# Optimization experiments

Measured on AMD Instinct MI355X. Metric: run time of the kernel, lower is better.

The kernel has to match this reference:

```python
import jax, jax.numpy as jnp
import numpy as np

N = 100000   # nodes
E = 1600000  # edges (avg degree 16)
D = 64       # feature dim
LN_EPS = 1e-5


def setup_inputs() -> dict:
    key = jax.random.key(0)
    ks = jax.random.split(key, 12)
    s = 1.0 / np.sqrt(D)
    x = jax.random.normal(ks[0], (N, D), dtype=jnp.float32)
    edge_index = jax.random.randint(ks[1], (2, E), 0, N, dtype=jnp.int32)
    routing_factor = jax.random.uniform(ks[2], (E,), dtype=jnp.float32)
    return {
        "x": x,
        "edge_index": edge_index,
        "routing_factor": routing_factor,
        "W_phys": jax.random.normal(ks[3], (D, D), dtype=jnp.float32) * s,
        "W_neur": jax.random.normal(ks[4], (D, D), dtype=jnp.float32) * s,
        "att_w": jax.random.normal(ks[5], (2 * D,), dtype=jnp.float32) * s,
        "channel_fusion": jnp.float32(0.5),
        "mlp_w1": jax.random.normal(ks[6], (2 * D, D), dtype=jnp.float32) * s,
        "mlp_b1": jnp.zeros((2 * D,), dtype=jnp.float32),
        "mlp_w2": jax.random.normal(ks[7], (D, 2 * D), dtype=jnp.float32) / np.sqrt(2 * D),
        "mlp_b2": jnp.zeros((D,), dtype=jnp.float32),
        "ln1_g": jnp.ones((D,), dtype=jnp.float32),
        "ln1_b": jnp.zeros((D,), dtype=jnp.float32),
        "ln2_g": jnp.ones((D,), dtype=jnp.float32),
        "ln2_b": jnp.zeros((D,), dtype=jnp.float32),
    }


def _layernorm(h, g, b):
    mu = jnp.mean(h, axis=-1, keepdims=True)
    var = jnp.var(h, axis=-1, keepdims=True)
    return (h - mu) * jax.lax.rsqrt(var + LN_EPS) * g + b


def reference(x, edge_index, routing_factor, W_phys, W_neur, att_w,
              channel_fusion, mlp_w1, mlp_b1, mlp_w2, mlp_b2,
              ln1_g, ln1_b, ln2_g, ln2_b):
    src, dst = edge_index[0], edge_index[1]
    x_src = x[src]  # [E, D]
    # att(cat([x_src, x_dst])) == x_src @ w[:D] + x_dst @ w[D:]
    att_scores = x_src @ att_w[:D] + x[dst] @ att_w[D:]  # [E]
    # segment softmax over destination nodes (equivalent to per-node loop)
    seg_max = jax.ops.segment_max(att_scores, dst, num_segments=N)
    e = jnp.exp(att_scores - seg_max[dst])
    denom = jax.ops.segment_sum(e, dst, num_segments=N)
    att = e / denom[dst]  # [E]
    # dual-channel messages (dropout inactive at eval)
    phys = routing_factor[:, None] * (x_src @ W_phys.T)
    neur = x_src @ W_neur.T
    alpha = jax.nn.sigmoid(channel_fusion)
    messages = att[:, None] * (alpha * phys + (1.0 - alpha) * neur)  # [E, D]
    out = jax.ops.segment_sum(messages, dst, num_segments=N)  # [N, D]
    h = _layernorm(jax.nn.gelu(out, approximate=False) + x, ln1_g, ln1_b)
    m = jax.nn.gelu(h @ mlp_w1.T + mlp_b1, approximate=False) @ mlp_w2.T + mlp_b2
    return _layernorm(m + h, ln2_g, ln2_b)
```

## Files before the change

kernel.cpp:

```cpp
#include <hip/hip_runtime.h>
#include <math.h>

#define NN 100000
#define NE 1600000
#define DD 64
#define NBUK 782
#define TILE 8192
#define NTB ((NE + TILE - 1) / TILE)
#define BSTRIDE 3072
#define SCAP 3072

typedef __attribute__((ext_vector_type(8))) short short8;
typedef __attribute__((ext_vector_type(4))) float f32x4;
typedef __attribute__((ext_vector_type(4))) _Float16 h4;

__device__ __forceinline__ float gelu_exact(float v) {
    return 0.5f * v * (1.0f + erff(v * 0.7071067811865475f));
}

__device__ __forceinline__ unsigned short f2bf(float f) {
    unsigned u = __float_as_uint(f);
    return (unsigned short)((u + 0x7FFFu + ((u >> 16) & 1u)) >> 16);
}
__device__ __forceinline__ float bf2f(unsigned short h) {
    return __uint_as_float((unsigned)h << 16);
}
__device__ __forceinline__ void split8v(float4 x0, float4 x1, short8& hi, short8& lo) {
    float v[8] = {x0.x, x0.y, x0.z, x0.w, x1.x, x1.y, x1.z, x1.w};
    #pragma unroll
    for (int i = 0; i < 8; ++i) {
        unsigned short h = f2bf(v[i]);
        hi[i] = (short)h;
        lo[i] = (short)f2bf(v[i] - bf2f(h));
    }
}
__device__ __forceinline__ void lds_frag(const float* g, int row, int u0, int s,
                                         short8& hi, short8& lo) {
    float4 p0 = *(const float4*)&g[row * 64 + ((u0 ^ s) << 2)];
    float4 p1 = *(const float4*)&g[row * 64 + (((u0 + 1) ^ s) << 2)];
    split8v(p0, p1, hi, lo);
}

template<bool F16>
__global__ __launch_bounds__(256) void k01(
    const float* __restrict__ Wp, const float* __restrict__ Wn,
    const float* __restrict__ w1, const float* __restrict__ w2,
    const float* __restrict__ cf,
    unsigned short* __restrict__ wh, unsigned short* __restrict__ wl,
    const float* __restrict__ x, const float* __restrict__ attw,
    float* __restrict__ es1, _Float16* __restrict__ xh)
{
    if (blockIdx.x < 96) {
        int t = blockIdx.x * 256 + threadIdx.x;
        float alpha = 1.0f / (1.0f + __expf(-cf[0]));
        float beta  = 1.0f - alpha;
        float v;
        if (t < 8192) {
            int d = t >> 7, k = t & 127;
            v = (k < 64) ? alpha * Wp[d * 64 + k] : beta * Wn[d * 64 + (k - 64)];
        } else if (t < 16384) {
            v = w1[t - 8192];
        } else {
            v = w2[t - 16384];
        }
        unsigned short h = f2bf(v);
        wh[t] = h;
        wl[t] = f2bf(v - bf2f(h));
    } else {
        int n = (blockIdx.x - 96) * 256 + threadIdx.x;
        if (n >= NN) return;
        const float4* x4 = (const float4*)(x + (size_t)n * DD);
        float a = 0.f;
        #pragma unroll
        for (int i = 0; i < DD/4; ++i) {
            float4 v = x4[i];
            a += v.x*attw[4*i+0] + v.y*attw[4*i+1] + v.z*attw[4*i+2] + v.w*attw[4*i+3];
            if (F16) {
                h4 hv = {(_Float16)v.x, (_Float16)v.y, (_Float16)v.z, (_Float16)v.w};
                *(h4*)(xh + (size_t)n * DD + 4*i) = hv;
            }
        }
        es1[n] = __expf(a);
    }
}

__global__ __launch_bounds__(1024) void ks_bscan(
    const int* __restrict__ bcount, int* __restrict__ bbase)
{
    __shared__ int sa[1024], sb[1024];
    int t = threadIdx.x;
    int v = (t < NBUK) ? bcount[t] : 0;
    sa[t] = v;
    __syncthreads();
    int* s = sa; int* d = sb;
    #pragma unroll
    for (int o = 1; o < 1024; o <<= 1) {
        d[t] = s[t] + ((t >= o) ? s[t - o] : 0);
        __syncthreads();
        int* tmp = s; s = d; d = tmp;
    }
    if (t < NBUK) bbase[t] = s[t] - v;
    if (t == 0) bbase[NBUK] = NE;
}

__global__ __launch_bounds__(256) void kscat1(
    const int* __restrict__ ei, const float* __restrict__ rf,
    int* __restrict__ bcount, uint2* __restrict__ tmp)
{
    __shared__ int hist[NBUK];
    __shared__ int gbase[NBUK];
    for (int i = threadIdx.x; i < NBUK; i += 256) hist[i] = 0;
    __syncthreads();
    int base = blockIdx.x * TILE;
    int end  = min(base + TILE, NE);
    for (int e = base + threadIdx.x; e < end; e += 256)
        atomicAdd(&hist[ei[NE + e] >> 7], 1);
    __syncthreads();
    for (int i = threadIdx.x; i < NBUK; i += 256) {
        int c = hist[i];
        gbase[i] = c ? (i * BSTRIDE + atomicAdd(bcount + i, c)) : 0;
        hist[i] = 0;
    }
    __syncthreads();
    for (int e = base + threadIdx.x; e < end; e += 256) {
        int src = ei[e];
        int dst = ei[NE + e];
        int b = dst >> 7;
        int t = atomicAdd(&hist[b], 1);
        tmp[gbase[b] + t] =
            make_uint2((unsigned)src | ((unsigned)(dst & 127) << 17),
                       __float_as_uint(rf[e]));
    }
}

__global__ __launch_bounds__(256) void kscat2(
    const uint2* __restrict__ tmp, const int* __restrict__ bcount,
    const int* __restrict__ bbase,
    int* __restrict__ off, uint2* __restrict__ sorted)
{
    __shared__ int hist[128], scn[128], tick[128];
    __shared__ uint2 obuf[SCAP];
    int b   = blockIdx.x;
    int tid = threadIdx.x;
    int si = b * BSTRIDE;
    int so = bbase[b];
    int m  = bcount[b];

    if (tid < 128) { hist[tid] = 0; tick[tid] = 0; }
    __syncthreads();

    for (int i = tid; i < m; i += 256)
        atomicAdd(&hist[tmp[si + i].x >> 17], 1);
    __syncthreads();

    if (tid < 128) scn[tid] = hist[tid];
    __syncthreads();
    #pragma unroll
    for (int o = 1; o < 128; o <<= 1) {
        int v = (tid < 128 && tid >= o) ? scn[tid - o] : 0;
        __syncthreads();
        if (tid < 128) scn[tid] += v;
        __syncthreads();
    }

    int nb0 = b * 128;
    if (tid < 128 && nb0 + tid < NN) off[nb0 + tid] = so + scn[tid] - hist[tid];
    if (b == NBUK - 1 && tid == 0) off[NN] = NE;
    __syncthreads();

    for (int i = tid; i < m; i += 256) {
        uint2 pr = tmp[si + i];
        int l = pr.x >> 17;
        int t = atomicAdd(&tick[l], 1);
        int lp = (scn[l] - hist[l]) + t;
        uint2 val = make_uint2(pr.x & 0x1FFFFu, pr.y);
        if (lp < SCAP) obuf[lp] = val;
        else sorted[so + lp] = val;
    }
    __syncthreads();
    int mm = min(m, SCAP);
    for (int i = tid; i < mm; i += 256)
        sorted[so + i] = obuf[i];
}

template<bool F16>
__global__ __launch_bounds__(256) void k4a_agg(
    const float2* __restrict__ sorted, const int* __restrict__ off,
    const float* __restrict__ es1,
    const float* __restrict__ x, const _Float16* __restrict__ xh,
    float* __restrict__ uv)
{
    int lane = threadIdx.x & 63;
    int n = blockIdx.x * 4 + (threadIdx.x >> 6);
    int r0 = off[n], r1 = off[n + 1];

    float den = 0.f, u = 0.f, v = 0.f;
    for (int base = r0; base < r1; base += 64) {
        int idx = base + lane;
        int cnt = min(64, r1 - base);
        int srcl = 0; float el = 0.f, efl = 0.f;
        if (idx < r1) {
            float2 p = sorted[idx];
            srcl = __float_as_int(p.x);
            el   = es1[srcl];
            efl  = el * p.y;
        }
        int j = 0;
        for (; j + 8 <= cnt; j += 8) {
            int a[8]; float e[8], f[8];
            #pragma unroll
            for (int t = 0; t < 8; ++t) {
                a[t] = __shfl(srcl, j + t);
                e[t] = __shfl(el,   j + t);
                f[t] = __shfl(efl,  j + t);
            }
            float xv[8];
            #pragma unroll
            for (int t = 0; t < 8; ++t)
                xv[t] = F16 ? (float)xh[(size_t)a[t] * DD + lane]
                            : x[(size_t)a[t] * DD + lane];
            #pragma unroll
            for (int t = 0; t < 8; ++t) {
                den += e[t];
                v += e[t] * xv[t];
                u += f[t] * xv[t];
            }
        }
        for (; j < cnt; ++j) {
            int   sj = __shfl(srcl, j);
            float ej = __shfl(el,   j);
            float fj = __shfl(efl,  j);
            float xv = F16 ? (float)xh[(size_t)sj * DD + lane]
                           : x[(size_t)sj * DD + lane];
            den += ej;
            v += ej * xv;
            u += fj * xv;
        }
    }
    float inv = (r1 > r0) ? 1.f / den : 0.f;
    uv[(size_t)n * 2*DD + lane]      = u * inv;
    uv[(size_t)n * 2*DD + DD + lane] = v * inv;
}

__global__ __launch_bounds__(512, 4) void k4b5(
    const float* __restrict__ uv,
    const unsigned short* __restrict__ wh, const unsigned short* __restrict__ wl,
    const float* __restrict__ x,
    const float* __restrict__ g1, const float* __restrict__ be1,
    const float* __restrict__ bb1, const float* __restrict__ bb2,
    const float* __restrict__ g2, const float* __restrict__ be2,
    float* __restrict__ out)
{
    __shared__ unsigned short WH[8192], WL[8192];
    __shared__ unsigned short W2H[4096], W2L[4096];
    __shared__ float Gt[8][1024];

    int tid  = threadIdx.x;
    int lane = tid & 63;
    int wv   = tid >> 6;
    int quad = lane >> 4, l16 = lane & 15;
    int s7   = l16 & 7;
    int nb = blockIdx.x * 128 + wv * 16;
    float* gt = Gt[wv];

    const float4* arow4 = (const float4*)(uv + (size_t)min(nb + l16, NN - 1) * 128);
    float4 av[8];
    #pragma unroll
    for (int ks = 0; ks < 4; ++ks) {
        av[2*ks]   = arow4[ks*8 + quad*2];
        av[2*ks+1] = arow4[ks*8 + quad*2 + 1];
    }
    float xr[4][4];
    #pragma unroll
    for (int r = 0; r < 4; ++r) {
        size_t nld = (size_t)min(nb + quad*4 + r, NN - 1) * 64;
        #pragma unroll
        for (int nt = 0; nt < 4; ++nt) xr[r][nt] = x[nld + nt*16 + l16];
    }

    #pragma unroll
    for (int k = 0; k < 2; ++k) {
        int i = tid + k*512;
        int row = i >> 4, u = i & 15;
        int up = u ^ (row & 7);
        *(short8*)&WH[row*128 + up*8] = *(const short8*)&wh[i*8];
        *(short8*)&WL[row*128 + up*8] = *(const short8*)&wl[i*8];
    }
    __syncthreads();

    f32x4 acc0[4] = {};
    #pragma unroll
    for (int ks = 0; ks < 4; ++ks) {
        short8 ah, al;
        split8v(av[2*ks], av[2*ks+1], ah, al);
        int u0 = 4*ks + quad;
        #pragma unroll
        for (int nt = 0; nt < 4; ++nt) {
            int wo = (nt*16 + l16)*128 + (u0 ^ s7)*8;
            short8 bh = *(const short8*)&WH[wo];
            short8 bl = *(const short8*)&WL[wo];
            acc0[nt] = __builtin_amdgcn_mfma_f32_16x16x32_bf16(ah, bh, acc0[nt], 0, 0, 0);
            acc0[nt] = __builtin_amdgcn_mfma_f32_16x16x32_bf16(al, bh, acc0[nt], 0, 0, 0);
            acc0[nt] = __builtin_amdgcn_mfma_f32_16x16x32_bf16(ah, bl, acc0[nt], 0, 0, 0);
        }
    }

    float hn[4][4];
    #pragma unroll
    for (int r = 0; r < 4; ++r) {
        float hv[4];
        #pragma unroll
        for (int nt = 0; nt < 4; ++nt)
            hv[nt] = gelu_exact(acc0[nt][r]) + xr[r][nt];
        float s = hv[0] + hv[1] + hv[2] + hv[3];
        #pragma unroll
        for (int o = 1; o < 16; o <<= 1) s += __shfl_xor(s, o);
        float mu = s * (1.0f/64.0f);
        float q = 0.f;
        #pragma unroll
        for (int nt = 0; nt < 4; ++nt) { float t = hv[nt] - mu; q += t*t; }
        #pragma unroll
        for (int o = 1; o < 16; o <<= 1) q += __shfl_xor(q, o);
        float rs = rsqrtf(q * (1.0f/64.0f) + 1e-5f);
        int row = quad*4 + r;
        #pragma unroll
        for (int nt = 0; nt < 4; ++nt) {
            int c = nt*16 + l16;
            float h = (hv[nt] - mu) * rs * g1[c] + be1[c];
            hn[r][nt] = h;
            int u = c >> 2;
            gt[row*64 + ((u ^ (row & 7)) << 2) + (c & 3)] = h;
        }
    }
    __syncthreads();

    #pragma unroll
    for (int k = 0; k < 2; ++k) {
        int i = tid + k*512;
        int row = i >> 3, u = i & 7;
        int up = u ^ (row & 7);
        *(short8*)&WH[row*64 + up*8] = *(const short8*)&wh[8192 + i*8];
        *(short8*)&WL[row*64 + up*8] = *(const short8*)&wl[8192 + i*8];
    }
    {
        int row = tid >> 3, u = tid & 7;
        int up = u ^ (row & 7);
        *(short8*)&W2H[row*64 + up*8] = *(const short8*)&wh[16384 + row*128 + u*8];
        *(short8*)&W2L[row*64 + up*8] = *(const short8*)&wl[16384 + row*128 + u*8];
    }
    __syncthreads();

    short8 ah1[2], al1[2];
    #pragma unroll
    for (int ks = 0; ks < 2; ++ks)
        lds_frag(gt, l16, 8*ks + 2*quad, s7, ah1[ks], al1[ks]);

    f32x4 acc2[4] = {};
    #pragma unroll
    for (int half = 0; half < 2; ++half) {
        f32x4 a1[4] = {};
        #pragma unroll
        for (int ks = 0; ks < 2; ++ks) {
            int u0 = 4*ks + quad;
            #pragma unroll
            for (int t = 0; t < 4; ++t) {
                int row = half*64 + t*16 + l16;
                int wo = row*64 + ((u0 ^ s7))*8;
                short8 bh = *(const short8*)&WH[wo];
                short8 bl = *(const short8*)&WL[wo];
                a1[t] = __builtin_amdgcn_mfma_f32_16x16x32_bf16(ah1[ks], bh, a1[t], 0, 0, 0);
                a1[t] = __builtin_amdgcn_mfma_f32_16x16x32_bf16(al1[ks], bh, a1[t], 0, 0, 0);
                a1[t] = __builtin_amdgcn_mfma_f32_16x16x32_bf16(ah1[ks], bl, a1[t], 0, 0, 0);
            }
        }
        #pragma unroll
        for (int t = 0; t < 4; ++t) {
            float b1v = bb1[half*64 + t*16 + l16];
            #pragma unroll
            for (int r = 0; r < 4; ++r) {
                int row = quad*4 + r;
                int c = t*16 + l16;
                int u = c >> 2;
                gt[row*64 + ((u ^ (row & 7)) << 2) + (c & 3)] = gelu_exact(a1[t][r] + b1v);
            }
        }
        #pragma unroll
        for (int ks2 = 0; ks2 < 2; ++ks2) {
            short8 ah2, al2;
            lds_frag(gt, l16, 8*ks2 + 2*quad, s7, ah2, al2);
            int u0 = 4*ks2 + quad;
            #pragma unroll
            for (int nt2 = 0; nt2 < 4; ++nt2) {
                int wo = (nt2*16 + l16)*64 + (u0 ^ s7)*8;
                short8 bh = *(const short8*)&W2H[wo];
                short8 bl = *(const short8*)&W2L[wo];
                acc2[nt2] = __builtin_amdgcn_mfma_f32_16x16x32_bf16(ah2, bh, acc2[nt2], 0, 0, 0);
                acc2[nt2] = __builtin_amdgcn_mfma_f32_16x16x32_bf16(al2, bh, acc2[nt2], 0, 0, 0);
                acc2[nt2] = __builtin_amdgcn_mfma_f32_16x16x32_bf16(ah2, bl, acc2[nt2], 0, 0, 0);
            }
        }
        if (half == 0) {
            __syncthreads();
            int row = tid >> 3, u = tid & 7;
            int up = u ^ (row & 7);
            *(short8*)&W2H[row*64 + up*8] = *(const short8*)&wh[16384 + row*128 + 64 + u*8];
            *(short8*)&W2L[row*64 + up*8] = *(const short8*)&wl[16384 + row*128 + 64 + u*8];
            __syncthreads();
        }
    }

    #pragma unroll
    for (int r = 0; r < 4; ++r) {
        int n = nb + quad * 4 + r;
        float mv[4];
        #pragma unroll
        for (int nt = 0; nt < 4; ++nt)
            mv[nt] = acc2[nt][r] + hn[r][nt] + bb2[nt*16 + l16];
        float s = mv[0] + mv[1] + mv[2] + mv[3];
        #pragma unroll
        for (int o = 1; o < 16; o <<= 1) s += __shfl_xor(s, o);
        float mu = s * (1.0f/64.0f);
        float q = 0.f;
        #pragma unroll
        for (int nt = 0; nt < 4; ++nt) { float t = mv[nt] - mu; q += t*t; }
        #pragma unroll
        for (int o = 1; o < 16; o <<= 1) q += __shfl_xor(q, o);
        float rs = rsqrtf(q * (1.0f/64.0f) + 1e-5f);
        if (n < NN) {
            #pragma unroll
            for (int nt = 0; nt < 4; ++nt) {
                int c = nt*16 + l16;
                out[(size_t)n * 64 + c] = (mv[nt] - mu) * rs * g2[c] + be2[c];
            }
        }
    }
}

extern "C" void kernel_launch(void* const* d_in, const int* in_sizes, int n_in,
                              void* d_out, int out_size, void* d_ws, size_t ws_size,
                              hipStream_t stream) {
    const float* x    = (const float*)d_in[0];
    const int*   ei   = (const int*)d_in[1];
    const float* rf   = (const float*)d_in[2];
    const float* Wp   = (const float*)d_in[3];
    const float* Wn   = (const float*)d_in[4];
    const float* attw = (const float*)d_in[5];
    const float* cf   = (const float*)d_in[6];
    const float* w1   = (const float*)d_in[7];
    const float* b1   = (const float*)d_in[8];
    const float* w2   = (const float*)d_in[9];
    const float* b2   = (const float*)d_in[10];
    const float* g1   = (const float*)d_in[11];
    const float* be1  = (const float*)d_in[12];
    const float* g2   = (const float*)d_in[13];
    const float* be2  = (const float*)d_in[14];
    float* out = (float*)d_out;

    float* ws = (float*)d_ws;
    float*  es1    = ws;
    float*  uv     = es1 + NN;
    unsigned short* wh = (unsigned short*)(uv + (size_t)NN * 128);
    unsigned short* wl = wh + 24576;
    uint2*  sorted = (uint2*)(wl + 24576);
    int*    off    = (int*)(sorted + NE);
    int*    bcount = off + NN + 1;
    int*    bbase  = bcount + NBUK;
    uintptr_t xp = ((uintptr_t)(bbase + NBUK + 1) + 15) & ~(uintptr_t)15;
    _Float16* xh = (_Float16*)xp;
    uint2*  tmp    = (uint2*)uv;

    size_t need = (size_t)((char*)(xh + (size_t)NN * DD) - (char*)d_ws);
    bool f16 = (ws_size >= need);

    hipMemsetAsync(bcount, 0, NBUK * sizeof(int), stream);

    int k01grid = 96 + (NN + 255) / 256;
    if (f16) k01<true>  <<<k01grid, 256, 0, stream>>>(Wp, Wn, w1, w2, cf, wh, wl, x, attw, es1, xh);
    else     k01<false> <<<k01grid, 256, 0, stream>>>(Wp, Wn, w1, w2, cf, wh, wl, x, attw, es1, xh);
    kscat1    <<<NTB, 256, 0, stream>>>(ei, rf, bcount, tmp);
    ks_bscan  <<<1, 1024, 0, stream>>>(bcount, bbase);
    kscat2    <<<NBUK, 256, 0, stream>>>(tmp, bcount, bbase, off, sorted);
    if (f16) k4a_agg<true>  <<<NN/4, 256, 0, stream>>>((const float2*)sorted, off, es1, x, xh, uv);
    else     k4a_agg<false> <<<NN/4, 256, 0, stream>>>((const float2*)sorted, off, es1, x, xh, uv);
    k4b5      <<<(NN+127)/128, 512, 0, stream>>>(uv, wh, wl, x, g1, be1, b1, b2, g2, be2, out);
}
```

Measured before the change: 300.7 us.

## Replace two-pass bucket sort with atomic counting sort and packed fp16 edge weights

Replaces the bucketed two-pass scatter with a per-node degree histogram (fused into k01), a three-kernel scan and a global-atomic scatter that writes edges directly to CSR slots. The scatter also precomputes exp(score) and exp*routing_factor and packs them as fp16 halves, so the aggregation kernel no longer gathers es1. Aggregation now reads edge records uniformly per wave and accumulates with packed fp16 dot2 instructions. This trades deterministic edge ordering and fp32 weights for fewer passes, with the risks of fp16 precision loss in exp weights (possible overflow) and contention on global atomics.

```diff
diff --git a/kernel.cpp b/kernel.cpp
--- a/kernel.cpp
+++ b/kernel.cpp
@@ -5,14 +5,12 @@
 #define NE 1600000
 #define DD 64
 #define NBUK 782
-#define TILE 8192
-#define NTB ((NE + TILE - 1) / TILE)
-#define BSTRIDE 3072
-#define SCAP 3072
+#define CNT_BLKS ((NE + 255) / 256)
 
 typedef __attribute__((ext_vector_type(8))) short short8;
 typedef __attribute__((ext_vector_type(4))) float f32x4;
 typedef __attribute__((ext_vector_type(4))) _Float16 h4;
+typedef __attribute__((ext_vector_type(2))) _Float16 f16x2;
 
 __device__ __forceinline__ float gelu_exact(float v) {
     return 0.5f * v * (1.0f + erff(v * 0.7071067811865475f));
@@ -41,17 +39,28 @@
     split8v(p0, p1, hi, lo);
 }
 
-template<bool F16>
+__device__ __forceinline__ f16x2 as_f16x2(unsigned int u) {
+    union { unsigned int x; f16x2 h; } c; c.x = u; return c.h;
+}
+__device__ __forceinline__ unsigned short h_as_us(_Float16 h) {
+    union { _Float16 h; unsigned short u; } c; c.h = h; return c.u;
+}
+__device__ __forceinline__ float us_as_f(unsigned short u) {
+    union { unsigned short u; _Float16 h; } c; c.u = u; return (float)c.h;
+}
+
 __global__ __launch_bounds__(256) void k01(
     const float* __restrict__ Wp, const float* __restrict__ Wn,
     const float* __restrict__ w1, const float* __restrict__ w2,
     const float* __restrict__ cf,
     unsigned short* __restrict__ wh, unsigned short* __restrict__ wl,
     const float* __restrict__ x, const float* __restrict__ attw,
-    float* __restrict__ es1, _Float16* __restrict__ xh)
-{
-    if (blockIdx.x < 96) {
-        int t = blockIdx.x * 256 + threadIdx.x;
+    float* __restrict__ es1, _Float16* __restrict__ xh,
+    const int* __restrict__ ei, int* __restrict__ cnt)
+{
+    int bid = blockIdx.x;
+    if (bid < 96) {
+        int t = bid * 256 + threadIdx.x;
         float alpha = 1.0f / (1.0f + __expf(-cf[0]));
         float beta  = 1.0f - alpha;
         float v;
@@ -66,8 +75,8 @@
         unsigned short h = f2bf(v);
         wh[t] = h;
         wl[t] = f2bf(v - bf2f(h));
-    } else {
-        int n = (blockIdx.x - 96) * 256 + threadIdx.x;
+    } else if (bid < 487) {
+        int n = (bid - 96) * 256 + threadIdx.x;
         if (n >= NN) return;
         const float4* x4 = (const float4*)(x + (size_t)n * DD);
         float a = 0.f;
@@ -75,21 +84,36 @@
         for (int i = 0; i < DD/4; ++i) {
             float4 v = x4[i];
             a += v.x*attw[4*i+0] + v.y*attw[4*i+1] + v.z*attw[4*i+2] + v.w*attw[4*i+3];
-            if (F16) {
-                h4 hv = {(_Float16)v.x, (_Float16)v.y, (_Float16)v.z, (_Float16)v.w};
-                *(h4*)(xh + (size_t)n * DD + 4*i) = hv;
-            }
+            h4 hv = {(_Float16)v.x, (_Float16)v.y, (_Float16)v.z, (_Float16)v.w};
+            *(h4*)(xh + (size_t)n * DD + 4*i) = hv;
         }
         es1[n] = __expf(a);
-    }
-}
-
-__global__ __launch_bounds__(1024) void ks_bscan(
-    const int* __restrict__ bcount, int* __restrict__ bbase)
+    } else {
+        int e = (bid - 487) * 256 + threadIdx.x;
+        if (e < NE) atomicAdd(&cnt[ei[NE + e]], 1);
+    }
+}
+
+__global__ __launch_bounds__(128) void kA(
+    const int* __restrict__ cnt, int* __restrict__ bsum)
+{
+    __shared__ int part[2];
+    int b = blockIdx.x, t = threadIdx.x;
+    int i = b * 128 + t;
+    int v = (i < NN) ? cnt[i] : 0;
+    #pragma unroll
+    for (int o = 32; o > 0; o >>= 1) v += __shfl_xor(v, o);
+    if ((t & 63) == 0) part[t >> 6] = v;
+    __syncthreads();
+    if (t == 0) bsum[b] = part[0] + part[1];
+}
+
+__global__ __launch_bounds__(1024) void kB(
+    const int* __restrict__ bsum, int* __restrict__ bbase)
 {
     __shared__ int sa[1024], sb[1024];
     int t = threadIdx.x;
-    int v = (t < NBUK) ? bcount[t] : 0;
+    int v = (t < NBUK) ? bsum[t] : 0;
     sa[t] = v;
     __syncthreads();
     int* s = sa; int* d = sb;
@@ -103,143 +127,100 @@
     if (t == 0) bbase[NBUK] = NE;
 }
 
-__global__ __launch_bounds__(256) void kscat1(
+__global__ __launch_bounds__(128) void kC(
+    const int* __restrict__ cnt, const int* __restrict__ bbase,
+    int* __restrict__ off, int* __restrict__ cur)
+{
+    __shared__ int w0tot;
+    int b = blockIdx.x, t = threadIdx.x;
+    int i = b * 128 + t;
+    int v = (i < NN) ? cnt[i] : 0;
+    int xsc = v;
+    #pragma unroll
+    for (int o = 1; o < 64; o <<= 1) {
+        int up = __shfl_up(xsc, o);
+        if ((t & 63) >= o) xsc += up;
+    }
+    if (t == 63) w0tot = xsc;
+    __syncthreads();
+    if (t >= 64) xsc += w0tot;
+    int excl = bbase[b] + xsc - v;
+    if (i < NN) { off[i] = excl; cur[i] = excl; }
+    if (b == NBUK - 1 && t == 127) off[NN] = NE;
+}
+
+__global__ __launch_bounds__(256) void kS(
     const int* __restrict__ ei, const float* __restrict__ rf,
-    int* __restrict__ bcount, uint2* __restrict__ tmp)
-{
-    __shared__ int hist[NBUK];
-    __shared__ int gbase[NBUK];
-    for (int i = threadIdx.x; i < NBUK; i += 256) hist[i] = 0;
-    __syncthreads();
-    int base = blockIdx.x * TILE;
-    int end  = min(base + TILE, NE);
-    for (int e = base + threadIdx.x; e < end; e += 256)
-        atomicAdd(&hist[ei[NE + e] >> 7], 1);
-    __syncthreads();
-    for (int i = threadIdx.x; i < NBUK; i += 256) {
-        int c = hist[i];
-        gbase[i] = c ? (i * BSTRIDE + atomicAdd(bcount + i, c)) : 0;
-        hist[i] = 0;
-    }
-    __syncthreads();
-    for (int e = base + threadIdx.x; e < end; e += 256) {
-        int src = ei[e];
-        int dst = ei[NE + e];
-        int b = dst >> 7;
-        int t = atomicAdd(&hist[b], 1);
-        tmp[gbase[b] + t] =
-            make_uint2((unsigned)src | ((unsigned)(dst & 127) << 17),
-                       __float_as_uint(rf[e]));
-    }
-}
-
-__global__ __launch_bounds__(256) void kscat2(
-    const uint2* __restrict__ tmp, const int* __restrict__ bcount,
-    const int* __restrict__ bbase,
-    int* __restrict__ off, uint2* __restrict__ sorted)
-{
-    __shared__ int hist[128], scn[128], tick[128];
-    __shared__ uint2 obuf[SCAP];
-    int b   = blockIdx.x;
-    int tid = threadIdx.x;
-    int si = b * BSTRIDE;
-    int so = bbase[b];
-    int m  = bcount[b];
-
-    if (tid < 128) { hist[tid] = 0; tick[tid] = 0; }
-    __syncthreads();
-
-    for (int i = tid; i < m; i += 256)
-        atomicAdd(&hist[tmp[si + i].x >> 17], 1);
-    __syncthreads();
-
-    if (tid < 128) scn[tid] = hist[tid];
-    __syncthreads();
-    #pragma unroll
-    for (int o = 1; o < 128; o <<= 1) {
-        int v = (tid < 128 && tid >= o) ? scn[tid - o] : 0;
-        __syncthreads();
-        if (tid < 128) scn[tid] += v;
-        __syncthreads();
-    }
-
-    int nb0 = b * 128;
-    if (tid < 128 && nb0 + tid < NN) off[nb0 + tid] = so + scn[tid] - hist[tid];
-    if (b == NBUK - 1 && tid == 0) off[NN] = NE;
-    __syncthreads();
-
-    for (int i = tid; i < m; i += 256) {
-        uint2 pr = tmp[si + i];
-        int l = pr.x >> 17;
-        int t = atomicAdd(&tick[l], 1);
-        int lp = (scn[l] - hist[l]) + t;
-        uint2 val = make_uint2(pr.x & 0x1FFFFu, pr.y);
-        if (lp < SCAP) obuf[lp] = val;
-        else sorted[so + lp] = val;
-    }
-    __syncthreads();
-    int mm = min(m, SCAP);
-    for (int i = tid; i < mm; i += 256)
-        sorted[so + i] = obuf[i];
-}
-
-template<bool F16>
+    const float* __restrict__ es1, int* __restrict__ cur,
+    uint2* __restrict__ sorted)
+{
+    int e = blockIdx.x * 256 + threadIdx.x;
+    if (e >= NE) return;
+    int src = ei[e];
+    int dst = ei[NE + e];
+    float es = es1[src];
+    float ef = es * rf[e];
+    unsigned packed = (unsigned)h_as_us((_Float16)es)
+                    | ((unsigned)h_as_us((_Float16)ef) << 16);
+    int p = atomicAdd(&cur[dst], 1);
+    sorted[p] = make_uint2((unsigned)src, packed);
+}
+
 __global__ __launch_bounds__(256) void k4a_agg(
-    const float2* __restrict__ sorted, const int* __restrict__ off,
-    const float* __restrict__ es1,
-    const float* __restrict__ x, const _Float16* __restrict__ xh,
-    float* __restrict__ uv)
+    const uint2* __restrict__ sorted, const int* __restrict__ off,
+    const _Float16* __restrict__ xh, float* __restrict__ uv)
 {
     int lane = threadIdx.x & 63;
     int n = blockIdx.x * 4 + (threadIdx.x >> 6);
-    int r0 = off[n], r1 = off[n + 1];
+    int r0 = __builtin_amdgcn_readfirstlane(off[n]);
+    int r1 = __builtin_amdgcn_readfirstlane(off[n + 1]);
+    const unsigned short* xs = (const unsigned short*)xh;
 
     float den = 0.f, u = 0.f, v = 0.f;
-    for (int base = r0; base < r1; base += 64) {
-        int idx = base + lane;
-        int cnt = min(64, r1 - base);
-        int srcl = 0; float el = 0.f, efl = 0.f;
-        if (idx < r1) {
-            float2 p = sorted[idx];
-            srcl = __float_as_int(p.x);
-            el   = es1[srcl];
-            efl  = el * p.y;
-        }
-        int j = 0;
-        for (; j + 8 <= cnt; j += 8) {
-            int a[8]; float e[8], f[8];
-            #pragma unroll
-            for (int t = 0; t < 8; ++t) {
-                a[t] = __shfl(srcl, j + t);
-                e[t] = __shfl(el,   j + t);
-                f[t] = __shfl(efl,  j + t);
-            }
-            float xv[8];
-            #pragma unroll
-            for (int t = 0; t < 8; ++t)
-                xv[t] = F16 ? (float)xh[(size_t)a[t] * DD + lane]
-                            : x[(size_t)a[t] * DD + lane];
-            #pragma unroll
-            for (int t = 0; t < 8; ++t) {
-                den += e[t];
-                v += e[t] * xv[t];
-                u += f[t] * xv[t];
-            }
-        }
-        for (; j < cnt; ++j) {
-            int   sj = __shfl(srcl, j);
-            float ej = __shfl(el,   j);
-            float fj = __shfl(efl,  j);
-            float xv = F16 ? (float)xh[(size_t)sj * DD + lane]
-                           : x[(size_t)sj * DD + lane];
-            den += ej;
-            v += ej * xv;
-            u += fj * xv;
-        }
+    const unsigned ONES = 0x3C003C00u;
+    int j = r0;
+    for (; j + 8 <= r1; j += 8) {
+        uint2 p[8];
+        #pragma unroll
+        for (int t = 0; t < 8; ++t) p[t] = sorted[j + t];
+        unsigned xv[4];
+        #pragma unroll
+        for (int q = 0; q < 4; ++q) {
+            unsigned a0 = xs[(size_t)p[2*q].x   * DD + lane];
+            unsigned a1 = xs[(size_t)p[2*q+1].x * DD + lane];
+            xv[q] = a0 | (a1 << 16);
+        }
+        #pragma unroll
+        for (int q = 0; q < 4; ++q) {
+            unsigned y0 = p[2*q].y, y1 = p[2*q+1].y;
+            unsigned e2 = (y0 & 0xFFFFu) | (y1 << 16);
+            unsigned f2 = (y0 >> 16) | (y1 & 0xFFFF0000u);
+            v   = __builtin_amdgcn_fdot2(as_f16x2(xv[q]), as_f16x2(e2), v, false);
+            u   = __builtin_amdgcn_fdot2(as_f16x2(xv[q]), as_f16x2(f2), u, false);
+            den = __builtin_amdgcn_fdot2(as_f16x2(e2), as_f16x2(ONES), den, false);
+        }
+    }
+    for (; j + 2 <= r1; j += 2) {
+        uint2 p0 = sorted[j], p1 = sorted[j + 1];
+        unsigned a0 = xs[(size_t)p0.x * DD + lane];
+        unsigned a1 = xs[(size_t)p1.x * DD + lane];
+        unsigned xv = a0 | (a1 << 16);
+        unsigned e2 = (p0.y & 0xFFFFu) | (p1.y << 16);
+        unsigned f2 = (p0.y >> 16) | (p1.y & 0xFFFF0000u);
+        v   = __builtin_amdgcn_fdot2(as_f16x2(xv), as_f16x2(e2), v, false);
+        u   = __builtin_amdgcn_fdot2(as_f16x2(xv), as_f16x2(f2), u, false);
+        den = __builtin_amdgcn_fdot2(as_f16x2(e2), as_f16x2(ONES), den, false);
+    }
+    if (j < r1) {
+        uint2 p0 = sorted[j];
+        float xvf = us_as_f((unsigned short)xs[(size_t)p0.x * DD + lane]);
+        float e = us_as_f((unsigned short)(p0.y & 0xFFFFu));
+        float f = us_as_f((unsigned short)(p0.y >> 16));
+        den += e; v += e * xvf; u += f * xvf;
     }
     float inv = (r1 > r0) ? 1.f / den : 0.f;
-    uv[(size_t)n * 2*DD + lane]      = u * inv;
-    uv[(size_t)n * 2*DD + DD + lane] = v * inv;
+    uv[(size_t)n * 128 + lane]      = u * inv;
+    uv[(size_t)n * 128 + 64 + lane] = v * inv;
 }
 
 __global__ __launch_bounds__(512, 4) void k4b5(
@@ -463,24 +444,21 @@
     unsigned short* wl = wh + 24576;
     uint2*  sorted = (uint2*)(wl + 24576);
     int*    off    = (int*)(sorted + NE);
-    int*    bcount = off + NN + 1;
-    int*    bbase  = bcount + NBUK;
+    int*    cnt    = off + NN + 1;
+    int*    cur    = cnt + NN;
+    int*    bsum   = cur + NN;
+    int*    bbase  = bsum + NBUK;
     uintptr_t xp = ((uintptr_t)(bbase + NBUK + 1) + 15) & ~(uintptr_t)15;
     _Float16* xh = (_Float16*)xp;
-    uint2*  tmp    = (uint2*)uv;
-
-    size_t need = (size_t)((char*)(xh + (size_t)NN * DD) - (char*)d_ws);
-    bool f16 = (ws_size >= need);
-
-    hipMemsetAsync(bcount, 0, NBUK * sizeof(int), stream);
-
-    int k01grid = 96 + (NN + 255) / 256;
-    if (f16) k01<true>  <<<k01grid, 256, 0, stream>>>(Wp, Wn, w1, w2, cf, wh, wl, x, attw, es1, xh);
-    else     k01<false> <<<k01grid, 256, 0, stream>>>(Wp, Wn, w1, w2, cf, wh, wl, x, attw, es1, xh);
-    kscat1    <<<NTB, 256, 0, stream>>>(ei, rf, bcount, tmp);
-    ks_bscan  <<<1, 1024, 0, stream>>>(bcount, bbase);
-    kscat2    <<<NBUK, 256, 0, stream>>>(tmp, bcount, bbase, off, sorted);
-    if (f16) k4a_agg<true>  <<<NN/4, 256, 0, stream>>>((const float2*)sorted, off, es1, x, xh, uv);
-    else     k4a_agg<false> <<<NN/4, 256, 0, stream>>>((const float2*)sorted, off, es1, x, xh, uv);
-    k4b5      <<<(NN+127)/128, 512, 0, stream>>>(uv, wh, wl, x, g1, be1, b1, b2, g2, be2, out);
-}
+
+    hipMemsetAsync(cnt, 0, NN * sizeof(int), stream);
+
+    k01 <<<487 + CNT_BLKS, 256, 0, stream>>>(Wp, Wn, w1, w2, cf, wh, wl,
+                                             x, attw, es1, xh, ei, cnt);
+    kA  <<<NBUK, 128, 0, stream>>>(cnt, bsum);
+    kB  <<<1, 1024, 0, stream>>>(bsum, bbase);
+    kC  <<<NBUK, 128, 0, stream>>>(cnt, bbase, off, cur);
+    kS  <<<CNT_BLKS, 256, 0, stream>>>(ei, rf, es1, cur, sorted);
+    k4a_agg <<<NN/4, 256, 0, stream>>>(sorted, off, xh, uv);
+    k4b5    <<<(NN+127)/128, 512, 0, stream>>>(uv, wh, wl, x, g1, be1, b1, b2, g2, be2, out);
+}
```

Measured after the change: 377.8 us. +25.7%, slower.

## Precompute fp16 edge weights in scatter and use packed fdot2 aggregation

Applied to the files above, without the earlier changes.

The edge scatter now gathers exp(source score) and multiplies it by the routing factor, packing both as fp16 into the sorted edge record. The aggregation kernel no longer does a per-edge es1 gather or lane shuffles. It reads records uniformly per wave and accumulates pairs of edges with fp16 dot2 instructions. The scatter tile size is reduced for more blocks, and the fp32 fallback path is removed, so fp16 x storage is now assumed to fit in the workspace. Rounding the softmax weights to fp16 adds precision loss and a risk of overflow when exp(score) exceeds the fp16 range.

```diff
diff --git a/kernel.cpp b/kernel.cpp
--- a/kernel.cpp
+++ b/kernel.cpp
@@ -5,7 +5,7 @@
 #define NE 1600000
 #define DD 64
 #define NBUK 782
-#define TILE 8192
+#define TILE 2048
 #define NTB ((NE + TILE - 1) / TILE)
 #define BSTRIDE 3072
 #define SCAP 3072
@@ -13,6 +13,7 @@
 typedef __attribute__((ext_vector_type(8))) short short8;
 typedef __attribute__((ext_vector_type(4))) float f32x4;
 typedef __attribute__((ext_vector_type(4))) _Float16 h4;
+typedef __attribute__((ext_vector_type(2))) _Float16 f16x2;
 
 __device__ __forceinline__ float gelu_exact(float v) {
     return 0.5f * v * (1.0f + erff(v * 0.7071067811865475f));
@@ -41,7 +42,16 @@
     split8v(p0, p1, hi, lo);
 }
 
-template<bool F16>
+__device__ __forceinline__ f16x2 as_f16x2(unsigned int u) {
+    union { unsigned int x; f16x2 h; } c; c.x = u; return c.h;
+}
+__device__ __forceinline__ unsigned short h_as_us(_Float16 h) {
+    union { _Float16 h; unsigned short u; } c; c.h = h; return c.u;
+}
+__device__ __forceinline__ float us_as_f(unsigned short u) {
+    union { unsigned short u; _Float16 h; } c; c.u = u; return (float)c.h;
+}
+
 __global__ __launch_bounds__(256) void k01(
     const float* __restrict__ Wp, const float* __restrict__ Wn,
     const float* __restrict__ w1, const float* __restrict__ w2,
@@ -50,8 +60,9 @@
     const float* __restrict__ x, const float* __restrict__ attw,
     float* __restrict__ es1, _Float16* __restrict__ xh)
 {
-    if (blockIdx.x < 96) {
-        int t = blockIdx.x * 256 + threadIdx.x;
+    int bid = blockIdx.x;
+    if (bid < 96) {
+        int t = bid * 256 + threadIdx.x;
         float alpha = 1.0f / (1.0f + __expf(-cf[0]));
         float beta  = 1.0f - alpha;
         float v;
@@ -67,7 +78,7 @@
         wh[t] = h;
         wl[t] = f2bf(v - bf2f(h));
     } else {
-        int n = (blockIdx.x - 96) * 256 + threadIdx.x;
+        int n = (bid - 96) * 256 + threadIdx.x;
         if (n >= NN) return;
         const float4* x4 = (const float4*)(x + (size_t)n * DD);
         float a = 0.f;
@@ -75,10 +86,8 @@
         for (int i = 0; i < DD/4; ++i) {
             float4 v = x4[i];
             a += v.x*attw[4*i+0] + v.y*attw[4*i+1] + v.z*attw[4*i+2] + v.w*attw[4*i+3];
-            if (F16) {
-                h4 hv = {(_Float16)v.x, (_Float16)v.y, (_Float16)v.z, (_Float16)v.w};
-                *(h4*)(xh + (size_t)n * DD + 4*i) = hv;
-            }
+            h4 hv = {(_Float16)v.x, (_Float16)v.y, (_Float16)v.z, (_Float16)v.w};
+            *(h4*)(xh + (size_t)n * DD + 4*i) = hv;
         }
         es1[n] = __expf(a);
     }
@@ -105,6 +114,7 @@
 
 __global__ __launch_bounds__(256) void kscat1(
     const int* __restrict__ ei, const float* __restrict__ rf,
+    const float* __restrict__ es1,
     int* __restrict__ bcount, uint2* __restrict__ tmp)
 {
     __shared__ int hist[NBUK];
@@ -125,11 +135,14 @@
     for (int e = base + threadIdx.x; e < end; e += 256) {
         int src = ei[e];
         int dst = ei[NE + e];
+        float es = es1[src];
+        float ef = es * rf[e];
+        unsigned packed = (unsigned)h_as_us((_Float16)es)
+                        | ((unsigned)h_as_us((_Float16)ef) << 16);
         int b = dst >> 7;
         int t = atomicAdd(&hist[b], 1);
         tmp[gbase[b] + t] =
-            make_uint2((unsigned)src | ((unsigned)(dst & 127) << 17),
-                       __float_as_uint(rf[e]));
+            make_uint2((unsigned)src | ((unsigned)(dst & 127) << 17), packed);
     }
 }
 
@@ -183,63 +196,61 @@
         sorted[so + i] = obuf[i];
 }
 
-template<bool F16>
 __global__ __launch_bounds__(256) void k4a_agg(
-    const float2* __restrict__ sorted, const int* __restrict__ off,
-    const float* __restrict__ es1,
-    const float* __restrict__ x, const _Float16* __restrict__ xh,
-    float* __restrict__ uv)
+    const uint2* __restrict__ sorted, const int* __restrict__ off,
+    const _Float16* __restrict__ xh, float* __restrict__ uv)
 {
     int lane = threadIdx.x & 63;
     int n = blockIdx.x * 4 + (threadIdx.x >> 6);
-    int r0 = off[n], r1 = off[n + 1];
+    int r0 = __builtin_amdgcn_readfirstlane(off[n]);
+    int r1 = __builtin_amdgcn_readfirstlane(off[n + 1]);
+    const unsigned short* xs = (const unsigned short*)xh;
 
     float den = 0.f, u = 0.f, v = 0.f;
-    for (int base = r0; base < r1; base += 64) {
-        int idx = base + lane;
-        int cnt = min(64, r1 - base);
-        int srcl = 0; float el = 0.f, efl = 0.f;
-        if (idx < r1) {
-            float2 p = sorted[idx];
-            srcl = __float_as_int(p.x);
-            el   = es1[srcl];
-            efl  = el * p.y;
-        }
-        int j = 0;
-        for (; j + 8 <= cnt; j += 8) {
-            int a[8]; float e[8], f[8];
-            #pragma unroll
-            for (int t = 0; t < 8; ++t) {
-                a[t] = __shfl(srcl, j + t);
-                e[t] = __shfl(el,   j + t);
-                f[t] = __shfl(efl,  j + t);
-            }
-            float xv[8];
-            #pragma unroll
-            for (int t = 0; t < 8; ++t)
-                xv[t] = F16 ? (float)xh[(size_t)a[t] * DD + lane]
-                            : x[(size_t)a[t] * DD + lane];
-            #pragma unroll
-            for (int t = 0; t < 8; ++t) {
-                den += e[t];
-                v += e[t] * xv[t];
-                u += f[t] * xv[t];
-            }
-        }
-        for (; j < cnt; ++j) {
-            int   sj = __shfl(srcl, j);
-            float ej = __shfl(el,   j);
-            float fj = __shfl(efl,  j);
-            float xv = F16 ? (float)xh[(size_t)sj * DD + lane]
-                           : x[(size_t)sj * DD + lane];
-            den += ej;
-            v += ej * xv;
-            u += fj * xv;
-        }
+    const unsigned ONES = 0x3C003C00u;
+    int j = r0;
+    for (; j + 8 <= r1; j += 8) {
+        uint2 p[8];
+        #pragma unroll
+        for (int t = 0; t < 8; ++t) p[t] = sorted[j + t];
+        unsigned xv[4];
+        #pragma unroll
+        for (int q = 0; q < 4; ++q) {
+            unsigned a0 = xs[(size_t)p[2*q].x   * DD + lane];
+            unsigned a1 = xs[(size_t)p[2*q+1].x * DD + lane];
+            xv[q] = a0 | (a1 << 16);
+        }
+        #pragma unroll
+        for (int q = 0; q < 4; ++q) {
+            unsigned y0 = p[2*q].y, y1 = p[2*q+1].y;
+            unsigned e2 = (y0 & 0xFFFFu) | (y1 << 16);
+            unsigned f2 = (y0 >> 16) | (y1 & 0xFFFF0000u);
+            v   = __builtin_amdgcn_fdot2(as_f16x2(xv[q]), as_f16x2(e2), v, false);
+            u   = __builtin_amdgcn_fdot2(as_f16x2(xv[q]), as_f16x2(f2), u, false);
+            den = __builtin_amdgcn_fdot2(as_f16x2(e2), as_f16x2(ONES), den, false);
+        }
+    }
+    for (; j + 2 <= r1; j += 2) {
+        uint2 p0 = sorted[j], p1 = sorted[j + 1];
+        unsigned a0 = xs[(size_t)p0.x * DD + lane];
+        unsigned a1 = xs[(size_t)p1.x * DD + lane];
+        unsigned xv = a0 | (a1 << 16);
+        unsigned e2 = (p0.y & 0xFFFFu) | (p1.y << 16);
+        unsigned f2 = (p0.y >> 16) | (p1.y & 0xFFFF0000u);
+        v   = __builtin_amdgcn_fdot2(as_f16x2(xv), as_f16x2(e2), v, false);
+        u   = __builtin_amdgcn_fdot2(as_f16x2(xv), as_f16x2(f2), u, false);
+        den = __builtin_amdgcn_fdot2(as_f16x2(e2), as_f16x2(ONES), den, false);
+    }
+    if (j < r1) {
+        uint2 p0 = sorted[j];
+        float xvf = us_as_f((unsigned short)xs[(size_t)p0.x * DD + lane]);
+        float e = us_as_f((unsigned short)(p0.y & 0xFFFFu));
+        float f = us_as_f((unsigned short)(p0.y >> 16));
+        den += e; v += e * xvf; u += f * xvf;
     }
     float inv = (r1 > r0) ? 1.f / den : 0.f;
-    uv[(size_t)n * 2*DD + lane]      = u * inv;
-    uv[(size_t)n * 2*DD + DD + lane] = v * inv;
+    uv[(size_t)n * 128 + lane]      = u * inv;
+    uv[(size_t)n * 128 + 64 + lane] = v * inv;
 }
 
 __global__ __launch_bounds__(512, 4) void k4b5(
@@ -469,18 +480,13 @@
     _Float16* xh = (_Float16*)xp;
     uint2*  tmp    = (uint2*)uv;
 
-    size_t need = (size_t)((char*)(xh + (size_t)NN * DD) - (char*)d_ws);
-    bool f16 = (ws_size >= need);
-
     hipMemsetAsync(bcount, 0, NBUK * sizeof(int), stream);
 
     int k01grid = 96 + (NN + 255) / 256;
-    if (f16) k01<true>  <<<k01grid, 256, 0, stream>>>(Wp, Wn, w1, w2, cf, wh, wl, x, attw, es1, xh);
-    else     k01<false> <<<k01grid, 256, 0, stream>>>(Wp, Wn, w1, w2, cf, wh, wl, x, attw, es1, xh);
-    kscat1    <<<NTB, 256, 0, stream>>>(ei, rf, bcount, tmp);
+    k01       <<<k01grid, 256, 0, stream>>>(Wp, Wn, w1, w2, cf, wh, wl, x, attw, es1, xh);
+    kscat1    <<<NTB, 256, 0, stream>>>(ei, rf, es1, bcount, tmp);
     ks_bscan  <<<1, 1024, 0, stream>>>(bcount, bbase);
     kscat2    <<<NBUK, 256, 0, stream>>>(tmp, bcount, bbase, off, sorted);
-    if (f16) k4a_agg<true>  <<<NN/4, 256, 0, stream>>>((const float2*)sorted, off, es1, x, xh, uv);
-    else     k4a_agg<false> <<<NN/4, 256, 0, stream>>>((const float2*)sorted, off, es1, x, xh, uv);
+    k4a_agg   <<<NN/4, 256, 0, stream>>>(sorted, off, xh, uv);
     k4b5      <<<(NN+127)/128, 512, 0, stream>>>(uv, wh, wl, x, g1, be1, b1, b2, g2, be2, out);
 }
```

Measured after the change: 306.0 us. No clear change (+1.8%).
